# Kernel tuning notes

Measured on AMD Instinct MI355X. Metric: run time of the kernel, lower is better.

Reference implementation:

```python
import jax, jax.numpy as jnp
import numpy as np

E = 30000
NUM_BASIS = 10
CUTOFF = 4.0
HIDDEN = 16
WNUM = 9216  # 64*64 + 64*32 + 32*32 + 32*64
INV_S3 = 1.0 / np.sqrt(3.0)
PW0 = np.sqrt(1.0 / 96.0)  # component/element norm, out 0e (alpha=1, x=64+32)
PW1 = np.sqrt(3.0 / 96.0)  # out 1o (alpha=3, x=64+32)


def setup_inputs() -> dict:
    key = jax.random.key(0)
    ks = jax.random.split(key, 8)
    x = jax.random.normal(ks[0], (E, 160), jnp.float32)
    rel_pos_sh = jax.random.normal(ks[1], (E, 4), jnp.float32)
    # distances strictly inside (0, cutoff) so envelope 1/d is finite
    distance = (jax.random.uniform(ks[2], (E, 1), jnp.float32) * 0.99 + 0.005) * CUTOFF
    # Bessel frequencies: n*pi, n=1..num_basis (trainable param in PyG)
    freq = jnp.arange(1, NUM_BASIS + 1, dtype=jnp.float32) * jnp.pi
    lim1 = 1.0 / np.sqrt(NUM_BASIS)
    w1 = jax.random.uniform(ks[3], (NUM_BASIS, HIDDEN), jnp.float32, -lim1, lim1)
    b1 = jax.random.uniform(ks[4], (HIDDEN,), jnp.float32, -lim1, lim1)
    lim2 = 1.0 / np.sqrt(HIDDEN)
    w2 = jax.random.uniform(ks[5], (HIDDEN, WNUM), jnp.float32, -lim2, lim2)
    b2 = jax.random.uniform(ks[6], (WNUM,), jnp.float32, -lim2, lim2)
    return dict(x=x, rel_pos_sh=rel_pos_sh, distance=distance,
                freq=freq, w1=w1, b1=b1, w2=w2, b2=b2)


def _radial_weights(distance, freq, w1, b1, w2, b2):
    d = distance[:, 0] / CUTOFF  # [E]
    d5 = d ** 5
    env = (1.0 / d - 28.0 * d5 + 48.0 * d5 * d - 21.0 * d5 * d * d) * (d < 1.0).astype(d.dtype)
    basis = env[:, None] * jnp.sin(freq[None, :] * d[:, None])  # [E, num_basis]
    h = jax.nn.silu(basis @ w1 + b1)
    return h @ w2 + b2  # [E, 9216]


def _tp(x, rel_pos_sh, weights):
    # split per-edge weights into the 4 CG paths (e3nn instruction order)
    Wa = weights[:, 0:4096].reshape(E, 64, 64)      # (0e,0e)->0e
    Wb = weights[:, 4096:6144].reshape(E, 64, 32)   # (0e,1o)->1o
    Wc = weights[:, 6144:7168].reshape(E, 32, 32)   # (1o,0e)->1o
    Wd = weights[:, 7168:9216].reshape(E, 32, 64)   # (1o,1o)->0e
    x0 = x[:, :64]                     # [E,64]   64x0e
    x1 = x[:, 64:].reshape(E, 32, 3)   # [E,32,3] 32x1o
    sh0 = rel_pos_sh[:, 0]             # [E]
    sh1 = rel_pos_sh[:, 1:4]           # [E,3]
    out0 = PW0 * (jnp.einsum('euw,eu->ew', Wa, x0) * sh0[:, None]
                  + INV_S3 * jnp.einsum('euw,eum,em->ew', Wd, x1, sh1))
    out1 = PW1 * INV_S3 * (jnp.einsum('euw,eu,em->ewm', Wb, x0, sh1)
                           + jnp.einsum('euw,eum->ewm', Wc, x1) * sh0[:, None, None])
    return jnp.concatenate([out0, out1.reshape(E, 96)], axis=-1)  # [E,160]


def reference(x, rel_pos_sh, distance, freq, w1, b1, w2, b2):
    weights = _radial_weights(distance, freq, w1, b1, w2, b2)
    return _tp(x, rel_pos_sh, weights)
```

## Files before the change

### kernel.cpp

```cpp
#include <hip/hip_runtime.h>
#include <hip/hip_bf16.h>
#include <cstddef>

#define E_TOTAL 30000
#define INV_S3 0.57735026918962576f
#define PW0    0.10206207261596575f
#define PW1    0.17677669529663687f

typedef __attribute__((ext_vector_type(8))) short bf16x8;
typedef __attribute__((ext_vector_type(4))) float f32x4;

#define NA_SH (34*6*512)
#define NB_SH (17*4*512)
#define NC_SH (17*2*512)
#define NH_BLKS ((E_TOTAL + 255) / 256)
#define NB_BLKS ((NA_SH + NB_SH + NC_SH) / 256)

__device__ __forceinline__ short f2bf(float v) {
    union { __hip_bfloat16 h; short s; } u;
    u.h = __float2bfloat16(v);
    return u.s;
}
__device__ __forceinline__ f32x4 ld4(const float* p) {
    return *reinterpret_cast<const f32x4*>(p);
}

__global__ void prep_all(const float* __restrict__ dist, const float* __restrict__ freq,
                         const float* __restrict__ w1, const float* __restrict__ b1,
                         const float* __restrict__ w2, const float* __restrict__ b2,
                         float* __restrict__ h_out,
                         short* __restrict__ Ba, short* __restrict__ Bb, short* __restrict__ Bc)
{
    const float C1 = PW1 * INV_S3, C2 = PW0 * INV_S3;
    if (blockIdx.x < NH_BLKS) {
        int e = blockIdx.x * 256 + threadIdx.x;
        if (e >= E_TOTAL) return;
        float d  = dist[e] * 0.25f;
        float d2 = d * d, d5 = d2 * d2 * d;
        float env = 1.0f / d - 28.0f * d5 + 48.0f * d5 * d - 21.0f * d5 * d * d;
        env = (d < 1.0f) ? env : 0.0f;
        float basis[10];
#pragma unroll
        for (int k = 0; k < 10; ++k) basis[k] = env * sinf(freq[k] * d);
#pragma unroll
        for (int j = 0; j < 16; ++j) {
            float a = b1[j];
#pragma unroll
            for (int k = 0; k < 10; ++k) a = fmaf(basis[k], w1[k * 16 + j], a);
            h_out[(size_t)e * 16 + j] = a / (1.0f + __expf(-a));
        }
        return;
    }
    int idx = (blockIdx.x - NH_BLKS) * 256 + threadIdx.x;
    if (idx < NA_SH) {
        int b = idx & 7, lane = (idx >> 3) & 63, t2 = idx >> 9;
        int nt = t2 % 6, c = t2 / 6;
        int kg = lane >> 4, jc = lane & 15, w = nt * 16 + jc;
        int cc = (c < 17) ? c : c - 17;
        int u  = ((c < 17) ? 0 : 32) + kg * 8 + b;
        float v;
        if (w < 64) v = (cc < 16) ? PW0 * w2[cc * 9216 + u * 64 + w]
                                  : PW0 * b2[u * 64 + w];
        else { int wb = w - 64;
               v = (cc < 16) ? C1 * w2[cc * 9216 + 4096 + u * 32 + wb]
                             : C1 * b2[4096 + u * 32 + wb]; }
        Ba[idx] = f2bf(v);
    } else if (idx < NA_SH + NB_SH) {
        int i2 = idx - NA_SH;
        int b = i2 & 7, lane = (i2 >> 3) & 63, t2 = i2 >> 9;
        int nt = t2 & 3, c = t2 >> 2;
        int kg = lane >> 4, jc = lane & 15, w = nt * 16 + jc;
        int u = kg * 8 + b;
        float v = (c < 16) ? C2 * w2[c * 9216 + 7168 + u * 64 + w]
                           : C2 * b2[7168 + u * 64 + w];
        Bb[i2] = f2bf(v);
    } else if (idx < NA_SH + NB_SH + NC_SH) {
        int i2 = idx - NA_SH - NB_SH;
        int b = i2 & 7, lane = (i2 >> 3) & 63, t2 = i2 >> 9;
        int nt = t2 & 1, c = t2 >> 1;
        int kg = lane >> 4, jc = lane & 15, w = nt * 16 + jc;
        int u = kg * 8 + b;
        float v = (c < 16) ? C1 * w2[c * 9216 + 6144 + u * 32 + w]
                           : C1 * b2[6144 + u * 32 + w];
        Bc[i2] = f2bf(v);
    }
}

template<int NT>
__device__ __forceinline__ void run_phase1(const float* __restrict__ xa,
        const float* __restrict__ hreg, short* __restrict__ cbuf,
        const short* __restrict__ Bbase, int lane, f32x4 (&acc)[4][6])
{
    const int kg = lane >> 4, jc = lane & 15;
    const bf16x8* Bp = reinterpret_cast<const bf16x8*>(Bbase);
    bf16x8 bpre[NT];
#pragma unroll
    for (int nt = 0; nt < NT; ++nt) bpre[nt] = Bp[nt * 64 + lane];
#pragma unroll 1
    for (int c = 0; c < 17; ++c) {
        bf16x8 bcur[NT];
#pragma unroll
        for (int nt = 0; nt < NT; ++nt) bcur[nt] = bpre[nt];
        if (c < 16) {
#pragma unroll
            for (int nt = 0; nt < NT; ++nt) bpre[nt] = Bp[((c + 1) * NT + nt) * 64 + lane];
        }
        float hc = (c < 16) ? hreg[c] : 1.0f;
#pragma unroll
        for (int g = 0; g < 4; ++g) {
            bf16x8 fr;
#pragma unroll
            for (int b = 0; b < 8; ++b) fr[b] = f2bf(hc * xa[g * 8 + b]);
            *reinterpret_cast<bf16x8*>(cbuf + g * 528 + lane * 8) = fr;
        }
        bf16x8 af[4];
#pragma unroll
        for (int mt = 0; mt < 4; ++mt)
            af[mt] = *reinterpret_cast<const bf16x8*>(cbuf + kg * 528 + mt * 128 + jc * 8);
#pragma unroll
        for (int nt = 0; nt < NT; ++nt)
#pragma unroll
            for (int mt = 0; mt < 4; ++mt)
                acc[mt][nt] = __builtin_amdgcn_mfma_f32_16x16x32_bf16(af[mt], bcur[nt], acc[mt][nt], 0, 0, 0);
    }
}

__device__ __forceinline__ void load_gamma_feats(const float* __restrict__ x,
        const float* __restrict__ h_arr, const float (*ssh)[4], int e0, int et,
        int lane, float* __restrict__ x1s, float* __restrict__ hg, float& sh0g)
{
    const int kg = lane >> 4, jc = lane & 15;
    const int rowA = et * 16 + jc;
    const int eA = e0 + rowA;
    const bool v = eA < E_TOTAL;
    const float* xp = x + (size_t)eA * 160 + 64 + 24 * kg;
#pragma unroll
    for (int i = 0; i < 6; ++i) {
        f32x4 q = v ? ld4(xp + 4 * i) : f32x4{0.f, 0.f, 0.f, 0.f};
        x1s[4*i] = q[0]; x1s[4*i+1] = q[1]; x1s[4*i+2] = q[2]; x1s[4*i+3] = q[3];
    }
    const float* hp = h_arr + (size_t)eA * 16;
#pragma unroll
    for (int i = 0; i < 4; ++i) {
        f32x4 q = v ? ld4(hp + 4 * i) : f32x4{0.f, 0.f, 0.f, 0.f};
        hg[4*i] = q[0]; hg[4*i+1] = q[1]; hg[4*i+2] = q[2]; hg[4*i+3] = q[3];
    }
    sh0g = ssh[rowA][0];
}

__device__ __forceinline__ void run_gamma(const float* __restrict__ x1s,
        const float* __restrict__ hg, float sh0g, const short* __restrict__ Bc,
        int lane, f32x4 (&acc)[3][2])
{
    const bf16x8* Bp = reinterpret_cast<const bf16x8*>(Bc);
    bf16x8 bpre[2];
#pragma unroll
    for (int nt = 0; nt < 2; ++nt) bpre[nt] = Bp[nt * 64 + lane];
#pragma unroll 1
    for (int c = 0; c < 17; ++c) {
        bf16x8 bcur[2]; bcur[0] = bpre[0]; bcur[1] = bpre[1];
        if (c < 16) { bpre[0] = Bp[((c+1)*2    ) * 64 + lane];
                      bpre[1] = Bp[((c+1)*2 + 1) * 64 + lane]; }
        float coef = (c < 16) ? sh0g * hg[c] : sh0g;
        bf16x8 am[3];
#pragma unroll
        for (int m = 0; m < 3; ++m) {
#pragma unroll
            for (int b = 0; b < 8; ++b) am[m][b] = f2bf(coef * x1s[3 * b + m]);
        }
#pragma unroll
        for (int nt = 0; nt < 2; ++nt)
#pragma unroll
            for (int m = 0; m < 3; ++m)
                acc[m][nt] = __builtin_amdgcn_mfma_f32_16x16x32_bf16(am[m], bcur[nt], acc[m][nt], 0, 0, 0);
    }
}

__launch_bounds__(256, 2)
__global__ void conv_main(const float* __restrict__ x, const float* __restrict__ rp,
                          const float* __restrict__ h_arr,
                          const short* __restrict__ Ba, const short* __restrict__ Bb,
                          const short* __restrict__ Bc, float* __restrict__ out)
{
    __shared__ __align__(16) char smem[69632];
    float (*slabA0)[100] = reinterpret_cast<float(*)[100]>(smem);
    float (*slabA1)[100] = reinterpret_cast<float(*)[100]>(smem + 25600);
    float (*slabB)[68]   = reinterpret_cast<float(*)[68]>(smem + 51200);
    float (*ssh)[4]      = reinterpret_cast<float(*)[4]>(smem + 68608);

    const int t = threadIdx.x, lane = t & 63, wave = t >> 6;
    const int kg = lane >> 4, jc = lane & 15;
    const int e0 = blockIdx.x * 64;

    { int ee = t >> 2, c4 = t & 3;
      ssh[ee][c4] = (e0 + ee < E_TOTAL) ? rp[(size_t)(e0 + ee) * 4 + c4] : 0.f; }
    __syncthreads();

    f32x4 acc[4][6];
    f32x4 accg[3][2];
    float x1s[24], hg[16], sh0g = 0.f;

    if (wave < 3) {
#pragma unroll
        for (int i = 0; i < 4; ++i)
#pragma unroll
            for (int j = 0; j < 6; ++j) acc[i][j] = f32x4{0.f, 0.f, 0.f, 0.f};
        const int e = e0 + lane;
        const bool ev = e < E_TOTAL;
        float hreg[16], xa[32];
        const float* hp = h_arr + (size_t)e * 16;
#pragma unroll
        for (int i = 0; i < 4; ++i) {
            f32x4 q = ev ? ld4(hp + 4 * i) : f32x4{0.f, 0.f, 0.f, 0.f};
            hreg[4*i] = q[0]; hreg[4*i+1] = q[1]; hreg[4*i+2] = q[2]; hreg[4*i+3] = q[3];
        }
        if (wave < 2) {
            const float* xp = x + (size_t)e * 160 + wave * 32;
#pragma unroll
            for (int i = 0; i < 8; ++i) {
                f32x4 q = ev ? ld4(xp + 4 * i) : f32x4{0.f, 0.f, 0.f, 0.f};
                xa[4*i] = q[0]; xa[4*i+1] = q[1]; xa[4*i+2] = q[2]; xa[4*i+3] = q[3];
            }
        } else {
            float s1 = ssh[lane][1], s2 = ssh[lane][2], s3 = ssh[lane][3];
            const float* xp = x + (size_t)e * 160 + 64;
#pragma unroll
            for (int s = 0; s < 4; ++s) {
                float x1t[24];
#pragma unroll
                for (int i = 0; i < 6; ++i) {
                    f32x4 q = ev ? ld4(xp + 24 * s + 4 * i) : f32x4{0.f, 0.f, 0.f, 0.f};
                    x1t[4*i] = q[0]; x1t[4*i+1] = q[1]; x1t[4*i+2] = q[2]; x1t[4*i+3] = q[3];
                }
#pragma unroll
                for (int u = 0; u < 8; ++u)
                    xa[8*s+u] = x1t[3*u] * s1 + x1t[3*u+1] * s2 + x1t[3*u+2] * s3;
            }
        }
        short* cbuf = reinterpret_cast<short*>(smem + wave * 4224);
        if (wave == 0)      run_phase1<6>(xa, hreg, cbuf, Ba,                lane, acc);
        else if (wave == 1) run_phase1<6>(xa, hreg, cbuf, Ba + 17 * 6 * 512, lane, acc);
        else                run_phase1<4>(xa, hreg, cbuf, Bb,                lane, acc);
    } else {
#pragma unroll
        for (int i = 0; i < 3; ++i) { accg[i][0] = f32x4{0.f,0.f,0.f,0.f}; accg[i][1] = f32x4{0.f,0.f,0.f,0.f}; }
        load_gamma_feats(x, h_arr, ssh, e0, 3, lane, x1s, hg, sh0g);
        run_gamma(x1s, hg, sh0g, Bc, lane, accg);
    }
    __syncthreads();

    if (wave == 0) {
#pragma unroll
        for (int mt = 0; mt < 4; ++mt)
#pragma unroll
            for (int nt = 0; nt < 6; ++nt)
#pragma unroll
                for (int r = 0; r < 4; ++r)
                    slabA0[mt*16 + 4*kg + r][nt*16 + jc] = acc[mt][nt][r];
    } else if (wave == 1) {
#pragma unroll
        for (int mt = 0; mt < 4; ++mt)
#pragma unroll
            for (int nt = 0; nt < 6; ++nt)
#pragma unroll
                for (int r = 0; r < 4; ++r)
                    slabA1[mt*16 + 4*kg + r][nt*16 + jc] = acc[mt][nt][r];
    } else if (wave == 2) {
#pragma unroll
        for (int mt = 0; mt < 4; ++mt)
#pragma unroll
            for (int nt = 0; nt < 4; ++nt)
#pragma unroll
                for (int r = 0; r < 4; ++r)
                    slabB[mt*16 + 4*kg + r][nt*16 + jc] = acc[mt][nt][r];
    }
    if (wave < 3) load_gamma_feats(x, h_arr, ssh, e0, wave, lane, x1s, hg, sh0g);
    __syncthreads();

    if (wave < 3) {
#pragma unroll
        for (int i = 0; i < 3; ++i) { accg[i][0] = f32x4{0.f,0.f,0.f,0.f}; accg[i][1] = f32x4{0.f,0.f,0.f,0.f}; }
        run_gamma(x1s, hg, sh0g, Bc, lane, accg);
    } else {
        for (int row = 0; row < 64; ++row) {
            if (e0 + row >= E_TOTAL) break;
            float v = ssh[row][0] * (slabA0[row][lane] + slabA1[row][lane]) + slabB[row][lane];
            out[(size_t)(e0 + row) * 160 + lane] = v;
        }
    }

    {
        const int et = wave;
#pragma unroll
        for (int m = 0; m < 3; ++m)
#pragma unroll
            for (int nt = 0; nt < 2; ++nt)
#pragma unroll
                for (int r = 0; r < 4; ++r) {
                    int row = et * 16 + 4 * kg + r;
                    int w = nt * 16 + jc;
                    if (e0 + row < E_TOTAL) {
                        float tbv = slabA0[row][64 + w] + slabA1[row][64 + w];
                        out[(size_t)(e0 + row) * 160 + 64 + w * 3 + m] =
                            tbv * ssh[row][1 + m] + accg[m][nt][r];
                    }
                }
    }
}

extern "C" void kernel_launch(void* const* d_in, const int* in_sizes, int n_in,
                              void* d_out, int out_size, void* d_ws, size_t ws_size,
                              hipStream_t stream) {
    const float* x    = (const float*)d_in[0];
    const float* rp   = (const float*)d_in[1];
    const float* dist = (const float*)d_in[2];
    const float* freq = (const float*)d_in[3];
    const float* w1   = (const float*)d_in[4];
    const float* b1   = (const float*)d_in[5];
    const float* w2   = (const float*)d_in[6];
    const float* b2   = (const float*)d_in[7];
    float* out = (float*)d_out;

    float* h_arr = (float*)d_ws;
    short* Ba = (short*)((char*)d_ws + 1920000);
    short* Bb = Ba + NA_SH;
    short* Bc = Bb + NB_SH;

    prep_all<<<NH_BLKS + NB_BLKS, 256, 0, stream>>>(dist, freq, w1, b1, w2, b2,
                                                    h_arr, Ba, Bb, Bc);
    conv_main<<<(E_TOTAL + 63) / 64, 256, 0, stream>>>(x, rp, h_arr, Ba, Bb, Bc, out);
}
```

Measured before the change: 110.4 us.

## Give each wave its own 16 edges and run all paths without LDS slabs

The main kernel is reorganized so that each wave owns 16 edge rows and runs every tensor-product path (A, B and gamma) for those rows itself. This removes the shared-memory slabs, the cross-wave reduction and the extra block syncs, and allows the occupancy hint to rise to 3 blocks. The weight-packing kernel now stages one weight chunk per block in shared memory with coalesced float4 loads instead of scattered per-element gathers. In exchange each wave streams all B fragments from global/L2 without the prefetch double-buffering, so per-wave MFMA chains get longer and register pressure may rise.

```diff
diff --git a/kernel.cpp b/kernel.cpp
--- a/kernel.cpp
+++ b/kernel.cpp
@@ -13,8 +13,7 @@
 #define NA_SH (34*6*512)
 #define NB_SH (17*4*512)
 #define NC_SH (17*2*512)
-#define NH_BLKS ((E_TOTAL + 255) / 256)
-#define NB_BLKS ((NA_SH + NB_SH + NC_SH) / 256)
+#define NH_BLKS 118
 
 __device__ __forceinline__ short f2bf(float v) {
     union { __hip_bfloat16 h; short s; } u;
@@ -32,8 +31,9 @@
                          short* __restrict__ Ba, short* __restrict__ Bb, short* __restrict__ Bc)
 {
     const float C1 = PW1 * INV_S3, C2 = PW0 * INV_S3;
+    const int t = threadIdx.x;
     if (blockIdx.x < NH_BLKS) {
-        int e = blockIdx.x * 256 + threadIdx.x;
+        int e = blockIdx.x * 256 + t;
         if (e >= E_TOTAL) return;
         float d  = dist[e] * 0.25f;
         float d2 = d * d, d5 = d2 * d2 * d;
@@ -51,261 +51,193 @@
         }
         return;
     }
-    int idx = (blockIdx.x - NH_BLKS) * 256 + threadIdx.x;
-    if (idx < NA_SH) {
-        int b = idx & 7, lane = (idx >> 3) & 63, t2 = idx >> 9;
-        int nt = t2 % 6, c = t2 / 6;
-        int kg = lane >> 4, jc = lane & 15, w = nt * 16 + jc;
+    __shared__ float sw[3072];
+    int blk = blockIdx.x - NH_BLKS;
+    if (blk < 34) {
+        int c = blk;
         int cc = (c < 17) ? c : c - 17;
-        int u  = ((c < 17) ? 0 : 32) + kg * 8 + b;
-        float v;
-        if (w < 64) v = (cc < 16) ? PW0 * w2[cc * 9216 + u * 64 + w]
-                                  : PW0 * b2[u * 64 + w];
-        else { int wb = w - 64;
-               v = (cc < 16) ? C1 * w2[cc * 9216 + 4096 + u * 32 + wb]
-                             : C1 * b2[4096 + u * 32 + wb]; }
-        Ba[idx] = f2bf(v);
-    } else if (idx < NA_SH + NB_SH) {
-        int i2 = idx - NA_SH;
-        int b = i2 & 7, lane = (i2 >> 3) & 63, t2 = i2 >> 9;
-        int nt = t2 & 3, c = t2 >> 2;
-        int kg = lane >> 4, jc = lane & 15, w = nt * 16 + jc;
-        int u = kg * 8 + b;
-        float v = (c < 16) ? C2 * w2[c * 9216 + 7168 + u * 64 + w]
-                           : C2 * b2[7168 + u * 64 + w];
-        Bb[i2] = f2bf(v);
-    } else if (idx < NA_SH + NB_SH + NC_SH) {
-        int i2 = idx - NA_SH - NB_SH;
-        int b = i2 & 7, lane = (i2 >> 3) & 63, t2 = i2 >> 9;
-        int nt = t2 & 1, c = t2 >> 1;
-        int kg = lane >> 4, jc = lane & 15, w = nt * 16 + jc;
-        int u = kg * 8 + b;
-        float v = (c < 16) ? C1 * w2[c * 9216 + 6144 + u * 32 + w]
-                           : C1 * b2[6144 + u * 32 + w];
-        Bc[i2] = f2bf(v);
-    }
-}
-
-template<int NT>
-__device__ __forceinline__ void run_phase1(const float* __restrict__ xa,
-        const float* __restrict__ hreg, short* __restrict__ cbuf,
-        const short* __restrict__ Bbase, int lane, f32x4 (&acc)[4][6])
-{
-    const int kg = lane >> 4, jc = lane & 15;
-    const bf16x8* Bp = reinterpret_cast<const bf16x8*>(Bbase);
-    bf16x8 bpre[NT];
-#pragma unroll
-    for (int nt = 0; nt < NT; ++nt) bpre[nt] = Bp[nt * 64 + lane];
-#pragma unroll 1
-    for (int c = 0; c < 17; ++c) {
-        bf16x8 bcur[NT];
-#pragma unroll
-        for (int nt = 0; nt < NT; ++nt) bcur[nt] = bpre[nt];
-        if (c < 16) {
-#pragma unroll
-            for (int nt = 0; nt < NT; ++nt) bpre[nt] = Bp[((c + 1) * NT + nt) * 64 + lane];
-        }
-        float hc = (c < 16) ? hreg[c] : 1.0f;
-#pragma unroll
-        for (int g = 0; g < 4; ++g) {
+        int ubase = (c < 17) ? 0 : 32;
+        const float* src = (cc < 16) ? (w2 + (size_t)cc * 9216) : b2;
+        const float4* pA = reinterpret_cast<const float4*>(src + ubase * 64);
+        for (int i = t; i < 512; i += 256) reinterpret_cast<float4*>(sw)[i] = pA[i];
+        const float4* pB = reinterpret_cast<const float4*>(src + 4096 + ubase * 32);
+        if (t < 256) reinterpret_cast<float4*>(sw + 2048)[t] = pB[t];
+        __syncthreads();
+        for (int i = t; i < 384; i += 256) {
+            int nt = i >> 6, lane = i & 63, kg = lane >> 4, jc = lane & 15;
+            int w = nt * 16 + jc;
             bf16x8 fr;
 #pragma unroll
-            for (int b = 0; b < 8; ++b) fr[b] = f2bf(hc * xa[g * 8 + b]);
-            *reinterpret_cast<bf16x8*>(cbuf + g * 528 + lane * 8) = fr;
-        }
-        bf16x8 af[4];
-#pragma unroll
-        for (int mt = 0; mt < 4; ++mt)
-            af[mt] = *reinterpret_cast<const bf16x8*>(cbuf + kg * 528 + mt * 128 + jc * 8);
-#pragma unroll
-        for (int nt = 0; nt < NT; ++nt)
-#pragma unroll
-            for (int mt = 0; mt < 4; ++mt)
-                acc[mt][nt] = __builtin_amdgcn_mfma_f32_16x16x32_bf16(af[mt], bcur[nt], acc[mt][nt], 0, 0, 0);
-    }
-}
-
-__device__ __forceinline__ void load_gamma_feats(const float* __restrict__ x,
-        const float* __restrict__ h_arr, const float (*ssh)[4], int e0, int et,
-        int lane, float* __restrict__ x1s, float* __restrict__ hg, float& sh0g)
-{
-    const int kg = lane >> 4, jc = lane & 15;
-    const int rowA = et * 16 + jc;
-    const int eA = e0 + rowA;
-    const bool v = eA < E_TOTAL;
-    const float* xp = x + (size_t)eA * 160 + 64 + 24 * kg;
-#pragma unroll
-    for (int i = 0; i < 6; ++i) {
-        f32x4 q = v ? ld4(xp + 4 * i) : f32x4{0.f, 0.f, 0.f, 0.f};
-        x1s[4*i] = q[0]; x1s[4*i+1] = q[1]; x1s[4*i+2] = q[2]; x1s[4*i+3] = q[3];
-    }
-    const float* hp = h_arr + (size_t)eA * 16;
-#pragma unroll
-    for (int i = 0; i < 4; ++i) {
-        f32x4 q = v ? ld4(hp + 4 * i) : f32x4{0.f, 0.f, 0.f, 0.f};
-        hg[4*i] = q[0]; hg[4*i+1] = q[1]; hg[4*i+2] = q[2]; hg[4*i+3] = q[3];
-    }
-    sh0g = ssh[rowA][0];
-}
-
-__device__ __forceinline__ void run_gamma(const float* __restrict__ x1s,
-        const float* __restrict__ hg, float sh0g, const short* __restrict__ Bc,
-        int lane, f32x4 (&acc)[3][2])
-{
-    const bf16x8* Bp = reinterpret_cast<const bf16x8*>(Bc);
-    bf16x8 bpre[2];
-#pragma unroll
-    for (int nt = 0; nt < 2; ++nt) bpre[nt] = Bp[nt * 64 + lane];
-#pragma unroll 1
-    for (int c = 0; c < 17; ++c) {
-        bf16x8 bcur[2]; bcur[0] = bpre[0]; bcur[1] = bpre[1];
-        if (c < 16) { bpre[0] = Bp[((c+1)*2    ) * 64 + lane];
-                      bpre[1] = Bp[((c+1)*2 + 1) * 64 + lane]; }
-        float coef = (c < 16) ? sh0g * hg[c] : sh0g;
-        bf16x8 am[3];
-#pragma unroll
-        for (int m = 0; m < 3; ++m) {
-#pragma unroll
-            for (int b = 0; b < 8; ++b) am[m][b] = f2bf(coef * x1s[3 * b + m]);
-        }
-#pragma unroll
-        for (int nt = 0; nt < 2; ++nt)
-#pragma unroll
-            for (int m = 0; m < 3; ++m)
-                acc[m][nt] = __builtin_amdgcn_mfma_f32_16x16x32_bf16(am[m], bcur[nt], acc[m][nt], 0, 0, 0);
-    }
-}
-
-__launch_bounds__(256, 2)
+            for (int b = 0; b < 8; ++b) {
+                int u = kg * 8 + b;
+                float v = (w < 64) ? PW0 * sw[u * 64 + w]
+                                   : C1  * sw[2048 + u * 32 + (w - 64)];
+                fr[b] = f2bf(v);
+            }
+            *reinterpret_cast<bf16x8*>(Ba + ((size_t)(c * 6 + nt)) * 512 + lane * 8) = fr;
+        }
+    } else if (blk < 51) {
+        int c = blk - 34;
+        const float* src = (c < 16) ? (w2 + (size_t)c * 9216) : b2;
+        const float4* p = reinterpret_cast<const float4*>(src + 7168);
+        for (int i = t; i < 512; i += 256) reinterpret_cast<float4*>(sw)[i] = p[i];
+        __syncthreads();
+        {
+            int nt = t >> 6, lane = t & 63, kg = lane >> 4, jc = lane & 15;
+            int w = nt * 16 + jc;
+            bf16x8 fr;
+#pragma unroll
+            for (int b = 0; b < 8; ++b) { int u = kg * 8 + b; fr[b] = f2bf(C2 * sw[u * 64 + w]); }
+            *reinterpret_cast<bf16x8*>(Bb + ((size_t)(c * 4 + nt)) * 512 + lane * 8) = fr;
+        }
+    } else {
+        int c = blk - 51;
+        const float* src = (c < 16) ? (w2 + (size_t)c * 9216) : b2;
+        const float4* p = reinterpret_cast<const float4*>(src + 6144);
+        if (t < 256) reinterpret_cast<float4*>(sw)[t] = p[t];
+        __syncthreads();
+        if (t < 128) {
+            int nt = t >> 6, lane = t & 63, kg = lane >> 4, jc = lane & 15;
+            int w = nt * 16 + jc;
+            bf16x8 fr;
+#pragma unroll
+            for (int b = 0; b < 8; ++b) { int u = kg * 8 + b; fr[b] = f2bf(C1 * sw[u * 32 + w]); }
+            *reinterpret_cast<bf16x8*>(Bc + ((size_t)(c * 2 + nt)) * 512 + lane * 8) = fr;
+        }
+    }
+}
+
+__device__ __forceinline__ void mstep6(const bf16x8* __restrict__ Bp, int base, float hc,
+                                       const float (&xs)[8], int lane, f32x4 (&acc)[6]) {
+    bf16x8 af;
+#pragma unroll
+    for (int b = 0; b < 8; ++b) af[b] = f2bf(hc * xs[b]);
+#pragma unroll
+    for (int nt = 0; nt < 6; ++nt) {
+        bf16x8 bc = Bp[(size_t)(base + nt) * 64 + lane];
+        acc[nt] = __builtin_amdgcn_mfma_f32_16x16x32_bf16(af, bc, acc[nt], 0, 0, 0);
+    }
+}
+__device__ __forceinline__ void mstep4(const bf16x8* __restrict__ Bp, int base, float hc,
+                                       const float (&xs)[8], int lane, f32x4 (&acc)[4]) {
+    bf16x8 af;
+#pragma unroll
+    for (int b = 0; b < 8; ++b) af[b] = f2bf(hc * xs[b]);
+#pragma unroll
+    for (int nt = 0; nt < 4; ++nt) {
+        bf16x8 bc = Bp[(size_t)(base + nt) * 64 + lane];
+        acc[nt] = __builtin_amdgcn_mfma_f32_16x16x32_bf16(af, bc, acc[nt], 0, 0, 0);
+    }
+}
+__device__ __forceinline__ void gstep(const bf16x8* __restrict__ Bp, int base, float coef,
+                                      const float (&x1w)[24], int lane, f32x4 (&acc)[3][2]) {
+    bf16x8 am[3];
+#pragma unroll
+    for (int m = 0; m < 3; ++m)
+#pragma unroll
+        for (int b = 0; b < 8; ++b) am[m][b] = f2bf(coef * x1w[3 * b + m]);
+#pragma unroll
+    for (int nt = 0; nt < 2; ++nt) {
+        bf16x8 bc = Bp[(size_t)(base + nt) * 64 + lane];
+#pragma unroll
+        for (int m = 0; m < 3; ++m)
+            acc[m][nt] = __builtin_amdgcn_mfma_f32_16x16x32_bf16(am[m], bc, acc[m][nt], 0, 0, 0);
+    }
+}
+
+__launch_bounds__(256, 3)
 __global__ void conv_main(const float* __restrict__ x, const float* __restrict__ rp,
                           const float* __restrict__ h_arr,
                           const short* __restrict__ Ba, const short* __restrict__ Bb,
                           const short* __restrict__ Bc, float* __restrict__ out)
 {
-    __shared__ __align__(16) char smem[69632];
-    float (*slabA0)[100] = reinterpret_cast<float(*)[100]>(smem);
-    float (*slabA1)[100] = reinterpret_cast<float(*)[100]>(smem + 25600);
-    float (*slabB)[68]   = reinterpret_cast<float(*)[68]>(smem + 51200);
-    float (*ssh)[4]      = reinterpret_cast<float(*)[4]>(smem + 68608);
-
+    __shared__ float ssh[64][4];
     const int t = threadIdx.x, lane = t & 63, wave = t >> 6;
     const int kg = lane >> 4, jc = lane & 15;
     const int e0 = blockIdx.x * 64;
 
     { int ee = t >> 2, c4 = t & 3;
       ssh[ee][c4] = (e0 + ee < E_TOTAL) ? rp[(size_t)(e0 + ee) * 4 + c4] : 0.f; }
+
+    const int erow = wave * 16 + jc;
+    const size_t eA = (size_t)(e0 + erow);
+    const bool ev = (e0 + erow) < E_TOTAL;
+    const float* xp = x + eA * 160;
+    const float* hp = h_arr + eA * 16;
+
+    float h[16];
+#pragma unroll
+    for (int i = 0; i < 4; ++i) {
+        f32x4 q = ev ? ld4(hp + 4 * i) : f32x4{0.f, 0.f, 0.f, 0.f};
+        h[4*i] = q[0]; h[4*i+1] = q[1]; h[4*i+2] = q[2]; h[4*i+3] = q[3];
+    }
+    float x0lo[8], x0hi[8];
+#pragma unroll
+    for (int i = 0; i < 2; ++i) {
+        f32x4 q = ev ? ld4(xp + kg * 8 + 4 * i) : f32x4{0.f, 0.f, 0.f, 0.f};
+        x0lo[4*i] = q[0]; x0lo[4*i+1] = q[1]; x0lo[4*i+2] = q[2]; x0lo[4*i+3] = q[3];
+        f32x4 r = ev ? ld4(xp + 32 + kg * 8 + 4 * i) : f32x4{0.f, 0.f, 0.f, 0.f};
+        x0hi[4*i] = r[0]; x0hi[4*i+1] = r[1]; x0hi[4*i+2] = r[2]; x0hi[4*i+3] = r[3];
+    }
+    float x1w[24];
+#pragma unroll
+    for (int i = 0; i < 6; ++i) {
+        f32x4 q = ev ? ld4(xp + 64 + 24 * kg + 4 * i) : f32x4{0.f, 0.f, 0.f, 0.f};
+        x1w[4*i] = q[0]; x1w[4*i+1] = q[1]; x1w[4*i+2] = q[2]; x1w[4*i+3] = q[3];
+    }
     __syncthreads();
 
-    f32x4 acc[4][6];
-    f32x4 accg[3][2];
-    float x1s[24], hg[16], sh0g = 0.f;
-
-    if (wave < 3) {
-#pragma unroll
-        for (int i = 0; i < 4; ++i)
-#pragma unroll
-            for (int j = 0; j < 6; ++j) acc[i][j] = f32x4{0.f, 0.f, 0.f, 0.f};
-        const int e = e0 + lane;
-        const bool ev = e < E_TOTAL;
-        float hreg[16], xa[32];
-        const float* hp = h_arr + (size_t)e * 16;
-#pragma unroll
-        for (int i = 0; i < 4; ++i) {
-            f32x4 q = ev ? ld4(hp + 4 * i) : f32x4{0.f, 0.f, 0.f, 0.f};
-            hreg[4*i] = q[0]; hreg[4*i+1] = q[1]; hreg[4*i+2] = q[2]; hreg[4*i+3] = q[3];
-        }
-        if (wave < 2) {
-            const float* xp = x + (size_t)e * 160 + wave * 32;
-#pragma unroll
-            for (int i = 0; i < 8; ++i) {
-                f32x4 q = ev ? ld4(xp + 4 * i) : f32x4{0.f, 0.f, 0.f, 0.f};
-                xa[4*i] = q[0]; xa[4*i+1] = q[1]; xa[4*i+2] = q[2]; xa[4*i+3] = q[3];
+    const float sh0 = ssh[erow][0];
+    float z[8];
+    { float s1 = ssh[erow][1], s2 = ssh[erow][2], s3 = ssh[erow][3];
+#pragma unroll
+      for (int u = 0; u < 8; ++u)
+          z[u] = x1w[3*u] * s1 + x1w[3*u+1] * s2 + x1w[3*u+2] * s3; }
+
+    const bf16x8* BpA = reinterpret_cast<const bf16x8*>(Ba);
+    const bf16x8* BpB = reinterpret_cast<const bf16x8*>(Bb);
+    const bf16x8* BpC = reinterpret_cast<const bf16x8*>(Bc);
+
+    f32x4 accA[6] = {};
+#pragma unroll
+    for (int c = 0; c < 16; ++c) mstep6(BpA, c * 6, h[c], x0lo, lane, accA);
+    mstep6(BpA, 16 * 6, 1.0f, x0lo, lane, accA);
+#pragma unroll
+    for (int c = 0; c < 16; ++c) mstep6(BpA, (17 + c) * 6, h[c], x0hi, lane, accA);
+    mstep6(BpA, 33 * 6, 1.0f, x0hi, lane, accA);
+
+    f32x4 accB[4] = {};
+#pragma unroll
+    for (int c = 0; c < 16; ++c) mstep4(BpB, c * 4, h[c], z, lane, accB);
+    mstep4(BpB, 16 * 4, 1.0f, z, lane, accB);
+
+#pragma unroll
+    for (int nt = 0; nt < 4; ++nt)
+#pragma unroll
+        for (int r = 0; r < 4; ++r) {
+            int row = wave * 16 + 4 * kg + r;
+            if (e0 + row < E_TOTAL)
+                out[(size_t)(e0 + row) * 160 + nt * 16 + jc] =
+                    ssh[row][0] * accA[nt][r] + accB[nt][r];
+        }
+
+    f32x4 accG[3][2] = {};
+#pragma unroll
+    for (int c = 0; c < 16; ++c) gstep(BpC, c * 2, sh0 * h[c], x1w, lane, accG);
+    gstep(BpC, 16 * 2, sh0, x1w, lane, accG);
+
+#pragma unroll
+    for (int m = 0; m < 3; ++m)
+#pragma unroll
+        for (int nt = 0; nt < 2; ++nt)
+#pragma unroll
+            for (int r = 0; r < 4; ++r) {
+                int row = wave * 16 + 4 * kg + r;
+                int w = nt * 16 + jc;
+                if (e0 + row < E_TOTAL)
+                    out[(size_t)(e0 + row) * 160 + 64 + w * 3 + m] =
+                        accA[4 + nt][r] * ssh[row][1 + m] + accG[m][nt][r];
             }
-        } else {
-            float s1 = ssh[lane][1], s2 = ssh[lane][2], s3 = ssh[lane][3];
-            const float* xp = x + (size_t)e * 160 + 64;
-#pragma unroll
-            for (int s = 0; s < 4; ++s) {
-                float x1t[24];
-#pragma unroll
-                for (int i = 0; i < 6; ++i) {
-                    f32x4 q = ev ? ld4(xp + 24 * s + 4 * i) : f32x4{0.f, 0.f, 0.f, 0.f};
-                    x1t[4*i] = q[0]; x1t[4*i+1] = q[1]; x1t[4*i+2] = q[2]; x1t[4*i+3] = q[3];
-                }
-#pragma unroll
-                for (int u = 0; u < 8; ++u)
-                    xa[8*s+u] = x1t[3*u] * s1 + x1t[3*u+1] * s2 + x1t[3*u+2] * s3;
-            }
-        }
-        short* cbuf = reinterpret_cast<short*>(smem + wave * 4224);
-        if (wave == 0)      run_phase1<6>(xa, hreg, cbuf, Ba,                lane, acc);
-        else if (wave == 1) run_phase1<6>(xa, hreg, cbuf, Ba + 17 * 6 * 512, lane, acc);
-        else                run_phase1<4>(xa, hreg, cbuf, Bb,                lane, acc);
-    } else {
-#pragma unroll
-        for (int i = 0; i < 3; ++i) { accg[i][0] = f32x4{0.f,0.f,0.f,0.f}; accg[i][1] = f32x4{0.f,0.f,0.f,0.f}; }
-        load_gamma_feats(x, h_arr, ssh, e0, 3, lane, x1s, hg, sh0g);
-        run_gamma(x1s, hg, sh0g, Bc, lane, accg);
-    }
-    __syncthreads();
-
-    if (wave == 0) {
-#pragma unroll
-        for (int mt = 0; mt < 4; ++mt)
-#pragma unroll
-            for (int nt = 0; nt < 6; ++nt)
-#pragma unroll
-                for (int r = 0; r < 4; ++r)
-                    slabA0[mt*16 + 4*kg + r][nt*16 + jc] = acc[mt][nt][r];
-    } else if (wave == 1) {
-#pragma unroll
-        for (int mt = 0; mt < 4; ++mt)
-#pragma unroll
-            for (int nt = 0; nt < 6; ++nt)
-#pragma unroll
-                for (int r = 0; r < 4; ++r)
-                    slabA1[mt*16 + 4*kg + r][nt*16 + jc] = acc[mt][nt][r];
-    } else if (wave == 2) {
-#pragma unroll
-        for (int mt = 0; mt < 4; ++mt)
-#pragma unroll
-            for (int nt = 0; nt < 4; ++nt)
-#pragma unroll
-                for (int r = 0; r < 4; ++r)
-                    slabB[mt*16 + 4*kg + r][nt*16 + jc] = acc[mt][nt][r];
-    }
-    if (wave < 3) load_gamma_feats(x, h_arr, ssh, e0, wave, lane, x1s, hg, sh0g);
-    __syncthreads();
-
-    if (wave < 3) {
-#pragma unroll
-        for (int i = 0; i < 3; ++i) { accg[i][0] = f32x4{0.f,0.f,0.f,0.f}; accg[i][1] = f32x4{0.f,0.f,0.f,0.f}; }
-        run_gamma(x1s, hg, sh0g, Bc, lane, accg);
-    } else {
-        for (int row = 0; row < 64; ++row) {
-            if (e0 + row >= E_TOTAL) break;
-            float v = ssh[row][0] * (slabA0[row][lane] + slabA1[row][lane]) + slabB[row][lane];
-            out[(size_t)(e0 + row) * 160 + lane] = v;
-        }
-    }
-
-    {
-        const int et = wave;
-#pragma unroll
-        for (int m = 0; m < 3; ++m)
-#pragma unroll
-            for (int nt = 0; nt < 2; ++nt)
-#pragma unroll
-                for (int r = 0; r < 4; ++r) {
-                    int row = et * 16 + 4 * kg + r;
-                    int w = nt * 16 + jc;
-                    if (e0 + row < E_TOTAL) {
-                        float tbv = slabA0[row][64 + w] + slabA1[row][64 + w];
-                        out[(size_t)(e0 + row) * 160 + 64 + w * 3 + m] =
-                            tbv * ssh[row][1 + m] + accg[m][nt][r];
-                    }
-                }
-    }
 }
 
 extern "C" void kernel_launch(void* const* d_in, const int* in_sizes, int n_in,
@@ -326,7 +258,7 @@
     short* Bb = Ba + NA_SH;
     short* Bc = Bb + NB_SH;
 
-    prep_all<<<NH_BLKS + NB_BLKS, 256, 0, stream>>>(dist, freq, w1, b1, w2, b2,
-                                                    h_arr, Ba, Bb, Bc);
+    prep_all<<<NH_BLKS + 68, 256, 0, stream>>>(dist, freq, w1, b1, w2, b2,
+                                               h_arr, Ba, Bb, Bc);
     conv_main<<<(E_TOTAL + 63) / 64, 256, 0, stream>>>(x, rp, h_arr, Ba, Bb, Bc, out);
 }
```

Result: slower. 128.3 us (+16.3%).
